# Kernel optimization log

Hardware: AMD Instinct MI355X
Metric: run time of the kernel (lower is better)

Reference implementation:

```python
import jax, jax.numpy as jnp
import numpy as np
import math

B, S, H, NH = 2, 2048, 2048, 16
HD = H // NH
BASE = 10000.0


def _rope_tables():
    inv_freq = 1.0 / (BASE ** (np.arange(0, HD, 2, dtype=np.float32) / HD))
    t = np.arange(S, dtype=np.float32)
    freqs = np.einsum('i,j->ij', t, inv_freq)          # [S, HD/2]
    emb = np.concatenate([freqs, freqs], axis=-1)       # [S, HD]
    return jnp.asarray(np.cos(emb)), jnp.asarray(np.sin(emb))


def setup_inputs() -> dict:
    key = jax.random.key(0)
    ks = jax.random.split(key, 6)
    scale = 1.0 / math.sqrt(H)
    cos, sin = _rope_tables()
    causal = np.triu(np.full((S, S), -1e9, dtype=np.float32), k=1)
    attn_bias = jnp.broadcast_to(jnp.asarray(causal)[None, None], (B, 1, S, S))
    return {
        'hidden_states': jax.random.normal(ks[0], (B, S, H), jnp.float32),
        'masks': jnp.zeros((B, S, S), jnp.float32),
        'attn_bias': attn_bias,
        'cos': cos,
        'sin': sin,
        'wq': jax.random.normal(ks[1], (H, H), jnp.float32) * scale,
        'wk': jax.random.normal(ks[2], (H, H), jnp.float32) * scale,
        'wv': jax.random.normal(ks[3], (H, H), jnp.float32) * scale,
        'wo': jax.random.normal(ks[4], (H, H), jnp.float32) * scale,
        'position_ids': jnp.broadcast_to(jnp.arange(S, dtype=jnp.int64)[None], (B, S)),
    }


def _rotate_half(x):
    x1, x2 = x[..., : x.shape[-1] // 2], x[..., x.shape[-1] // 2:]
    return jnp.concatenate([-x2, x1], axis=-1)


def reference(hidden_states, masks, attn_bias, cos, sin, wq, wk, wv, wo, position_ids):
    b, s, h = hidden_states.shape
    nh, hd = NH, HD
    # QKV projections (torch Linear: x @ W.T), split heads -> [b, nh, s, hd]
    def proj(w):
        return (hidden_states @ w.T).reshape(b, s, nh, hd).transpose(0, 2, 1, 3)
    q, k, v = proj(wq), proj(wk), proj(wv)
    # RoPE
    cos_p = cos[position_ids][:, None]  # [b, 1, s, hd]
    sin_p = sin[position_ids][:, None]
    q = q * cos_p + _rotate_half(q) * sin_p
    k = k * cos_p + _rotate_half(k) * sin_p
    # attention scores with additive masks (mx_attn branch, fp math)
    att = jnp.einsum('bhqd,bhkd->bhqk', q / math.sqrt(hd), k)
    att = att + attn_bias + masks[:, None]
    att = jax.nn.softmax(att, axis=-1)
    out = jnp.einsum('bhqk,bhkd->bhqd', att, v)
    out = out.transpose(0, 2, 1, 3).reshape(b, s, h)
    return out @ wo.T
```

## Files before the change

### kernel.cpp

```cpp
#include <hip/hip_runtime.h>
#include <stdint.h>

#define B_  2
#define S_  2048
#define H_  2048
#define NH_ 16
#define HD_ 128

typedef __bf16 v8bf __attribute__((ext_vector_type(8)));
typedef float  v4f  __attribute__((ext_vector_type(4)));

__device__ __forceinline__ float b2f(unsigned short u) {
  union { unsigned int i; float f; } x; x.i = ((unsigned int)u) << 16; return x.f;
}
__device__ __forceinline__ unsigned short f2b(float f) {
  union { float f; unsigned int i; } x; x.f = f;
  unsigned int r = x.i + 0x7FFFu + ((x.i >> 16) & 1u);
  return (unsigned short)(r >> 16);
}

__device__ __forceinline__ void async16(const void* g, void* l) {
  __builtin_amdgcn_global_load_lds(
      (const __attribute__((address_space(1))) void*)g,
      (__attribute__((address_space(3))) void*)l, 16, 0, 0);
}

__global__ __launch_bounds__(256) void cvt_all(const float* __restrict__ hid,
                                               const float* __restrict__ wq,
                                               const float* __restrict__ wk,
                                               const float* __restrict__ wv,
                                               const float* __restrict__ wo,
                                               unsigned short* __restrict__ Xb,
                                               unsigned short* __restrict__ Wqb,
                                               unsigned short* __restrict__ Wkb,
                                               unsigned short* __restrict__ Wvb,
                                               unsigned short* __restrict__ Wob) {
  int bid = blockIdx.x;
  const float* src;
  unsigned short* dst;
  int rel;
  if (bid < 8192)       { src = hid; dst = Xb;  rel = bid; }
  else if (bid < 12288) { src = wq;  dst = Wqb; rel = bid - 8192; }
  else if (bid < 16384) { src = wk;  dst = Wkb; rel = bid - 12288; }
  else if (bid < 20480) { src = wv;  dst = Wvb; rel = bid - 16384; }
  else                  { src = wo;  dst = Wob; rel = bid - 20480; }
  int i = rel * 256 + threadIdx.x;
  float4 f = *(const float4*)(src + (size_t)i * 4);
  ushort4 u;
  u.x = f2b(f.x); u.y = f2b(f.y); u.z = f2b(f.z); u.w = f2b(f.w);
  *(ushort4*)(dst + (size_t)i * 4) = u;
}

__device__ __forceinline__ void gemm_tile_nt(const unsigned short* __restrict__ A,
                                             const unsigned short* __restrict__ Bm,
                                             int m0, int n0, int Kdim,
                                             unsigned short* As, unsigned short* Bs,
                                             v4f (&acc)[2][8]) {
  const int tid = threadIdx.x;
  const int lane = tid & 63, w = tid >> 6;
  const int lr = lane & 15, lg = lane >> 4;
  const int wm = w * 32;

  for (int k0 = 0; k0 < Kdim; k0 += 32) {
    __syncthreads();
#pragma unroll
    for (int i = 0; i < 2; ++i) {
      const int cbase = i * 256 + w * 64;
      const int cc = cbase + lane;
      const int row = cc >> 2, col = (cc & 3) << 3;
      async16(A  + (size_t)(m0 + row) * Kdim + k0 + col, (char*)As + (size_t)cbase * 16);
      async16(Bm + (size_t)(n0 + row) * Kdim + k0 + col, (char*)Bs + (size_t)cbase * 16);
    }
    __syncthreads();
    v8bf a[2], bb[8];
#pragma unroll
    for (int i = 0; i < 2; i++) a[i]  = *(const v8bf*)(As + (wm + i * 16 + lr) * 32 + lg * 8);
#pragma unroll
    for (int i = 0; i < 8; i++) bb[i] = *(const v8bf*)(Bs + (i * 16 + lr) * 32 + lg * 8);
#pragma unroll
    for (int mi = 0; mi < 2; mi++)
#pragma unroll
      for (int ni = 0; ni < 8; ni++)
        acc[mi][ni] = __builtin_amdgcn_mfma_f32_16x16x32_bf16(a[mi], bb[ni], acc[mi][ni], 0, 0, 0);
  }
}

__global__ __launch_bounds__(256, 2) void gemm_qkv(const unsigned short* __restrict__ X,
                                                   const unsigned short* __restrict__ Wq,
                                                   const unsigned short* __restrict__ Wk,
                                                   const unsigned short* __restrict__ Wv,
                                                   const float* __restrict__ cosT,
                                                   const float* __restrict__ sinT,
                                                   unsigned short* __restrict__ Qo,
                                                   unsigned short* __restrict__ Ko,
                                                   unsigned short* __restrict__ Vt) {
  __shared__ unsigned short As[128 * 32], Bs[128 * 32];
  const int m0 = blockIdx.x * 128;
  const int ny = blockIdx.y;
  const int sel = ny >> 4;
  const int h = ny & 15;
  const unsigned short* Bm = (sel == 0) ? Wq : (sel == 1 ? Wk : Wv);
  const int n0 = h * 128;

  v4f acc[2][8];
#pragma unroll
  for (int i = 0; i < 2; i++)
#pragma unroll
    for (int j = 0; j < 8; j++) { v4f z = {0.f, 0.f, 0.f, 0.f}; acc[i][j] = z; }

  gemm_tile_nt(X, Bm, m0, n0, H_, As, Bs, acc);

  const int lane = threadIdx.x & 63, w = threadIdx.x >> 6;
  const int lr = lane & 15, lg = lane >> 4;
  const int rbase = m0 + w * 32;

  if (sel < 2) {
    unsigned short* Out = (sel == 0) ? Qo : Ko;
    const float sc = (sel == 0) ? (float)(0.08838834764831845 * 1.4426950408889634) : 1.0f;
#pragma unroll
    for (int mi = 0; mi < 2; mi++)
#pragma unroll
      for (int ni = 0; ni < 4; ni++)
#pragma unroll
        for (int r = 0; r < 4; r++) {
          int row = rbase + mi * 16 + lg * 4 + r;
          int s = row & 2047;
          int d = ni * 16 + lr;
          float c  = cosT[(size_t)s * HD_ + d];
          float sn = sinT[(size_t)s * HD_ + d];
          float x1 = acc[mi][ni][r], x2 = acc[mi][ni + 4][r];
          Out[(size_t)row * H_ + n0 + d]      = f2b((x1 * c - x2 * sn) * sc);
          Out[(size_t)row * H_ + n0 + d + 64] = f2b((x2 * c + x1 * sn) * sc);
        }
  } else {
#pragma unroll
    for (int mi = 0; mi < 2; mi++)
#pragma unroll
      for (int ni = 0; ni < 8; ni++) {
        int row0 = rbase + mi * 16 + lg * 4;
        int b = row0 >> 11, s0 = row0 & 2047;
        int d = ni * 16 + lr;
        ushort4 u;
        u.x = f2b(acc[mi][ni][0]); u.y = f2b(acc[mi][ni][1]);
        u.z = f2b(acc[mi][ni][2]); u.w = f2b(acc[mi][ni][3]);
        *(ushort4*)(Vt + ((size_t)((b * NH_ + h) * HD_) + d) * S_ + s0) = u;
      }
  }
}

__global__ __launch_bounds__(256, 2) void gemm_out(const unsigned short* __restrict__ A,
                                                   const unsigned short* __restrict__ Wo,
                                                   float* __restrict__ Out) {
  __shared__ unsigned short As[128 * 32], Bs[128 * 32];
  const int m0 = blockIdx.x * 128;
  const int n0 = blockIdx.y * 128;

  v4f acc[2][8];
#pragma unroll
  for (int i = 0; i < 2; i++)
#pragma unroll
    for (int j = 0; j < 8; j++) { v4f z = {0.f, 0.f, 0.f, 0.f}; acc[i][j] = z; }

  gemm_tile_nt(A, Wo, m0, n0, H_, As, Bs, acc);

  const int lane = threadIdx.x & 63, w = threadIdx.x >> 6;
  const int lr = lane & 15, lg = lane >> 4;
#pragma unroll
  for (int mi = 0; mi < 2; mi++)
#pragma unroll
    for (int ni = 0; ni < 8; ni++)
#pragma unroll
      for (int r = 0; r < 4; r++)
        Out[(size_t)(m0 + w * 32 + mi * 16 + lg * 4 + r) * H_ + n0 + ni * 16 + lr] =
            acc[mi][ni][r];
}

#define KT_ 64

__global__ __launch_bounds__(512, 2) void attn_kernel(const unsigned short* __restrict__ Qb,
                                                      const unsigned short* __restrict__ Kb,
                                                      const unsigned short* __restrict__ Vt,
                                                      unsigned short* __restrict__ Ob) {
  __shared__ __align__(16) char smem[90112];
  unsigned short* Ps = (unsigned short*)(smem + 71680);

  const int tid = threadIdx.x, lane = tid & 63, w = tid >> 6;
  const int lr = lane & 15, lg = lane >> 4;
  const int qp = blockIdx.x, h = blockIdx.y, b = blockIdx.z;

  const int wtile = (w < 4) ? qp : (15 - qp);
  const int wrow = wtile * 128 + (w & 3) * 32;
  const int nkt = (16 - qp) * 2;

  auto stage = [&](int kt, char* Kd) {
    const int k0 = kt * KT_;
    char* Vd = Kd + 17408;
#pragma unroll
    for (int i = 0; i < 3; ++i) {
      int cbase = i * 512 + w * 64;
      if (cbase < 1088) {
        int cc = cbase + lane;
        int row = cc / 17, pos = cc % 17;
        int p2 = (pos == 16) ? 0 : pos;
        async16(Kb + (size_t)(b * S_ + k0 + row) * H_ + h * HD_ + p2 * 8,
                Kd + (size_t)cbase * 16);
      }
    }
#pragma unroll
    for (int i = 0; i < 3; ++i) {
      int cbase = i * 512 + w * 64;
      if (cbase < 1152) {
        int cc = cbase + lane;
        int row = cc / 9, pos = cc % 9;
        int p2 = (pos == 8) ? 0 : pos;
        async16(Vt + ((size_t)((b * NH_ + h) * HD_ + row)) * S_ + k0 + p2 * 8,
                Vd + (size_t)cbase * 16);
      }
    }
  };

  v8bf qf[2][4];
#pragma unroll
  for (int mt = 0; mt < 2; mt++)
#pragma unroll
    for (int ks = 0; ks < 4; ks++)
      qf[mt][ks] = *(const v8bf*)(Qb + (size_t)(b * S_ + wrow + mt * 16 + lr) * H_ +
                                  h * HD_ + ks * 32 + lg * 8);

  v4f o[2][8];
#pragma unroll
  for (int mt = 0; mt < 2; mt++)
#pragma unroll
    for (int nt = 0; nt < 8; nt++) { v4f z = {0.f, 0.f, 0.f, 0.f}; o[mt][nt] = z; }
  float mst[2][4], lst[2][4];
#pragma unroll
  for (int mt = 0; mt < 2; mt++)
#pragma unroll
    for (int r = 0; r < 4; r++) { mst[mt][r] = -1e30f; lst[mt][r] = 0.f; }

  stage(0, smem);
  __syncthreads();

  int cur = 0;
  for (int kt = 0; kt < nkt; kt++) {
    char* curb = smem + cur * 35840;
    if (kt + 1 < nkt) stage(kt + 1, smem + (cur ^ 1) * 35840);

    unsigned short* Ks = (unsigned short*)curb;
    unsigned short* Vs = (unsigned short*)(curb + 17408);
    const int k0 = kt * KT_;

    if (k0 <= wrow + 31) {
      v4f sacc[2][4];
#pragma unroll
      for (int mt = 0; mt < 2; mt++)
#pragma unroll
        for (int nt = 0; nt < 4; nt++) { v4f z = {0.f, 0.f, 0.f, 0.f}; sacc[mt][nt] = z; }
#pragma unroll
      for (int nt = 0; nt < 4; nt++) {
        v8bf kf[4];
#pragma unroll
        for (int ks = 0; ks < 4; ks++)
          kf[ks] = *(const v8bf*)(Ks + (nt * 16 + lr) * 136 + ks * 32 + lg * 8);
#pragma unroll
        for (int mt = 0; mt < 2; mt++)
#pragma unroll
          for (int ks = 0; ks < 4; ks++)
            sacc[mt][nt] =
                __builtin_amdgcn_mfma_f32_16x16x32_bf16(qf[mt][ks], kf[ks], sacc[mt][nt], 0, 0, 0);
      }
      if (k0 + KT_ - 1 > wrow) {
#pragma unroll
        for (int mt = 0; mt < 2; mt++)
#pragma unroll
          for (int nt = 0; nt < 4; nt++)
#pragma unroll
            for (int r = 0; r < 4; r++) {
              int key = k0 + nt * 16 + lr;
              int query = wrow + mt * 16 + lg * 4 + r;
              if (key > query) sacc[mt][nt][r] = -1e30f;
            }
      }
#pragma unroll
      for (int mt = 0; mt < 2; mt++) {
        float rmax[4], alpha[4], rsum[4];
#pragma unroll
        for (int r = 0; r < 4; r++) {
          float v = fmaxf(fmaxf(sacc[mt][0][r], sacc[mt][1][r]),
                          fmaxf(sacc[mt][2][r], sacc[mt][3][r]));
#pragma unroll
          for (int off = 8; off >= 1; off >>= 1) v = fmaxf(v, __shfl_xor(v, off, 64));
          rmax[r] = v;
        }
#pragma unroll
        for (int r = 0; r < 4; r++) {
          float mnew = fmaxf(mst[mt][r], rmax[r]);
          alpha[r] = exp2f(mst[mt][r] - mnew);
          mst[mt][r] = mnew;
          rsum[r] = 0.f;
        }
#pragma unroll
        for (int nt = 0; nt < 4; nt++)
#pragma unroll
          for (int r = 0; r < 4; r++) {
            float p = exp2f(sacc[mt][nt][r] - mst[mt][r]);
            sacc[mt][nt][r] = p;
            rsum[r] += p;
          }
#pragma unroll
        for (int r = 0; r < 4; r++) {
#pragma unroll
          for (int off = 8; off >= 1; off >>= 1) rsum[r] += __shfl_xor(rsum[r], off, 64);
          lst[mt][r] = lst[mt][r] * alpha[r] + rsum[r];
        }
#pragma unroll
        for (int nt = 0; nt < 8; nt++)
#pragma unroll
          for (int r = 0; r < 4; r++) o[mt][nt][r] *= alpha[r];
      }
      v8bf bv[8][2];
#pragma unroll
      for (int nt = 0; nt < 8; nt++)
#pragma unroll
        for (int ks = 0; ks < 2; ks++)
          bv[nt][ks] = *(const v8bf*)(Vs + (nt * 16 + lr) * 72 + ks * 32 + lg * 8);
#pragma unroll
      for (int mt = 0; mt < 2; mt++) {
#pragma unroll
        for (int nt = 0; nt < 4; nt++)
#pragma unroll
          for (int r = 0; r < 4; r++) {
            union { float f; unsigned u; } pu; pu.f = sacc[mt][nt][r];
            Ps[w * 1152 + (lg * 4 + r) * 72 + nt * 16 + lr] =
                (unsigned short)(pu.u >> 16);
          }
        asm volatile("" ::: "memory");
        v8bf af[2];
#pragma unroll
        for (int ks = 0; ks < 2; ks++)
          af[ks] = *(const v8bf*)(Ps + w * 1152 + lr * 72 + ks * 32 + lg * 8);
#pragma unroll
        for (int nt = 0; nt < 8; nt++)
#pragma unroll
          for (int ks = 0; ks < 2; ks++)
            o[mt][nt] = __builtin_amdgcn_mfma_f32_16x16x32_bf16(af[ks], bv[nt][ks], o[mt][nt], 0, 0, 0);
        asm volatile("" ::: "memory");
      }
    }
    __syncthreads();
    cur ^= 1;
  }
#pragma unroll
  for (int mt = 0; mt < 2; mt++) {
    float inv[4];
#pragma unroll
    for (int r = 0; r < 4; r++) inv[r] = 1.f / lst[mt][r];
#pragma unroll
    for (int nt = 0; nt < 8; nt++)
#pragma unroll
      for (int r = 0; r < 4; r++) {
        int row = wrow + mt * 16 + lg * 4 + r;
        int col = h * HD_ + nt * 16 + lr;
        Ob[(size_t)(b * S_ + row) * H_ + col] = f2b(o[mt][nt][r] * inv[r]);
      }
  }
}

extern "C" void kernel_launch(void* const* d_in, const int* in_sizes, int n_in,
                              void* d_out, int out_size, void* d_ws, size_t ws_size,
                              hipStream_t stream) {
  const float* hidden = (const float*)d_in[0];
  const float* cosT = (const float*)d_in[3];
  const float* sinT = (const float*)d_in[4];
  const float* wq = (const float*)d_in[5];
  const float* wk = (const float*)d_in[6];
  const float* wv = (const float*)d_in[7];
  const float* wo = (const float*)d_in[8];
  float* out = (float*)d_out;

  char* p = (char*)d_ws;
  const size_t SZ_X = (size_t)4096 * 2048 * 2;
  const size_t SZ_W = (size_t)2048 * 2048 * 2;
  unsigned short* Xb  = (unsigned short*)p; p += SZ_X;
  unsigned short* Wqb = (unsigned short*)p; p += SZ_W;
  unsigned short* Wkb = (unsigned short*)p; p += SZ_W;
  unsigned short* Wvb = (unsigned short*)p; p += SZ_W;
  unsigned short* Wob = (unsigned short*)p; p += SZ_W;
  unsigned short* Qb  = (unsigned short*)p; p += SZ_X;
  unsigned short* Kb  = (unsigned short*)p; p += SZ_X;
  unsigned short* Vt  = (unsigned short*)p; p += SZ_X;
  unsigned short* Ob  = (unsigned short*)p; p += SZ_X;

  cvt_all<<<24576, 256, 0, stream>>>(hidden, wq, wk, wv, wo, Xb, Wqb, Wkb, Wvb, Wob);
  gemm_qkv<<<dim3(32, 48), 256, 0, stream>>>(Xb, Wqb, Wkb, Wvb, cosT, sinT, Qb, Kb, Vt);
  attn_kernel<<<dim3(8, 16, 2), 512, 0, stream>>>(Qb, Kb, Vt, Ob);
  gemm_out<<<dim3(32, 16), 256, 0, stream>>>(Ob, Wob, out);
}
```

Measured before the change: 448.6 us.

## Rewrite QKV GEMM with 256x256 tiles, double-buffered swizzled LDS, and interleaved MFMA

```diff
diff --git a/kernel.cpp b/kernel.cpp
--- a/kernel.cpp
+++ b/kernel.cpp
@@ -85,7 +85,7 @@
   }
 }
 
-__global__ __launch_bounds__(256, 2) void gemm_qkv(const unsigned short* __restrict__ X,
+__global__ __launch_bounds__(512, 2) void gemm_qkv(const unsigned short* __restrict__ X,
                                                    const unsigned short* __restrict__ Wq,
                                                    const unsigned short* __restrict__ Wk,
                                                    const unsigned short* __restrict__ Wv,
@@ -94,50 +94,151 @@
                                                    unsigned short* __restrict__ Qo,
                                                    unsigned short* __restrict__ Ko,
                                                    unsigned short* __restrict__ Vt) {
-  __shared__ unsigned short As[128 * 32], Bs[128 * 32];
-  const int m0 = blockIdx.x * 128;
+  __shared__ __align__(16) unsigned short lds[4][256 * 64];
+
+  const int tid = threadIdx.x, lane = tid & 63, w = tid >> 6;
+  const int lr = lane & 15, lg = lane >> 4;
+  const int wm = w >> 1, wn = w & 1;
+  const int m0 = blockIdx.x * 256;
   const int ny = blockIdx.y;
-  const int sel = ny >> 4;
-  const int h = ny & 15;
-  const unsigned short* Bm = (sel == 0) ? Wq : (sel == 1 ? Wk : Wv);
-  const int n0 = h * 128;
-
-  v4f acc[2][8];
-#pragma unroll
-  for (int i = 0; i < 2; i++)
+  const int sel = ny >> 3;
+  const int nt = ny & 7;
+  const int n0 = nt * 256;
+  const unsigned short* Bw = (sel == 0) ? Wq : (sel == 1 ? Wk : Wv);
+  const int xsw = (lr & 7) << 3;
+
+  auto stg = [&](const unsigned short* G, int g0, int k0, unsigned short* dst) {
+#pragma unroll
+    for (int i = 0; i < 4; ++i) {
+      const int cbase = i * 512 + w * 64;
+      const int cc = cbase + lane;
+      const int row = cc >> 3;
+      const int kq = (cc & 7) ^ (row & 7);
+      async16(G + (size_t)(g0 + row) * H_ + k0 + kq * 8, (char*)dst + (size_t)cbase * 16);
+    }
+  };
+
+  v4f acc[4][8];
+#pragma unroll
+  for (int i = 0; i < 4; i++)
 #pragma unroll
     for (int j = 0; j < 8; j++) { v4f z = {0.f, 0.f, 0.f, 0.f}; acc[i][j] = z; }
 
-  gemm_tile_nt(X, Bm, m0, n0, H_, As, Bs, acc);
-
-  const int lane = threadIdx.x & 63, w = threadIdx.x >> 6;
-  const int lr = lane & 15, lg = lane >> 4;
-  const int rbase = m0 + w * 32;
-
+  stg(X,  m0, 0, lds[0]);
+  stg(Bw, n0, 0, lds[1]);
+  __syncthreads();
+
+  for (int t = 0; t < 32; ++t) {
+    const unsigned short* As = lds[(t & 1) * 2];
+    const unsigned short* Bs = lds[(t & 1) * 2 + 1];
+    unsigned short* Ad = lds[((t + 1) & 1) * 2];
+    unsigned short* Bd = lds[((t + 1) & 1) * 2 + 1];
+    const int kn = (t + 1) * 64;
+    v8bf bf[8][2], af[2];
+
+    if (t < 31) stg(X, m0, kn, Ad);
+#pragma unroll
+    for (int ni = 0; ni < 8; ni++) {
+      const unsigned short* rp = Bs + (size_t)(wn * 128 + ni * 16 + lr) * 64;
+      bf[ni][0] = *(const v8bf*)(rp + ((lg * 8) ^ xsw));
+      bf[ni][1] = *(const v8bf*)(rp + ((32 + lg * 8) ^ xsw));
+    }
+    {
+      const unsigned short* rp = As + (size_t)(wm * 64 + lr) * 64;
+      af[0] = *(const v8bf*)(rp + ((lg * 8) ^ xsw));
+      af[1] = *(const v8bf*)(rp + ((32 + lg * 8) ^ xsw));
+    }
+    __builtin_amdgcn_s_barrier();
+    asm volatile("s_waitcnt lgkmcnt(0)" ::: "memory");
+    __builtin_amdgcn_sched_barrier(0);
+    __builtin_amdgcn_s_setprio(1);
+#pragma unroll
+    for (int ni = 0; ni < 8; ni++) {
+      acc[0][ni] = __builtin_amdgcn_mfma_f32_16x16x32_bf16(af[0], bf[ni][0], acc[0][ni], 0, 0, 0);
+      acc[0][ni] = __builtin_amdgcn_mfma_f32_16x16x32_bf16(af[1], bf[ni][1], acc[0][ni], 0, 0, 0);
+    }
+    __builtin_amdgcn_s_setprio(0);
+    __builtin_amdgcn_s_barrier();
+
+    if (t < 31) stg(Bw, n0, kn, Bd);
+    {
+      const unsigned short* rp = As + (size_t)(wm * 64 + 16 + lr) * 64;
+      af[0] = *(const v8bf*)(rp + ((lg * 8) ^ xsw));
+      af[1] = *(const v8bf*)(rp + ((32 + lg * 8) ^ xsw));
+    }
+    __builtin_amdgcn_s_barrier();
+    asm volatile("s_waitcnt lgkmcnt(0)" ::: "memory");
+    __builtin_amdgcn_sched_barrier(0);
+    __builtin_amdgcn_s_setprio(1);
+#pragma unroll
+    for (int ni = 0; ni < 8; ni++) {
+      acc[1][ni] = __builtin_amdgcn_mfma_f32_16x16x32_bf16(af[0], bf[ni][0], acc[1][ni], 0, 0, 0);
+      acc[1][ni] = __builtin_amdgcn_mfma_f32_16x16x32_bf16(af[1], bf[ni][1], acc[1][ni], 0, 0, 0);
+    }
+    __builtin_amdgcn_s_setprio(0);
+    __builtin_amdgcn_s_barrier();
+
+    {
+      const unsigned short* rp = As + (size_t)(wm * 64 + 32 + lr) * 64;
+      af[0] = *(const v8bf*)(rp + ((lg * 8) ^ xsw));
+      af[1] = *(const v8bf*)(rp + ((32 + lg * 8) ^ xsw));
+    }
+    __builtin_amdgcn_s_barrier();
+    asm volatile("s_waitcnt lgkmcnt(0)" ::: "memory");
+    __builtin_amdgcn_sched_barrier(0);
+    __builtin_amdgcn_s_setprio(1);
+#pragma unroll
+    for (int ni = 0; ni < 8; ni++) {
+      acc[2][ni] = __builtin_amdgcn_mfma_f32_16x16x32_bf16(af[0], bf[ni][0], acc[2][ni], 0, 0, 0);
+      acc[2][ni] = __builtin_amdgcn_mfma_f32_16x16x32_bf16(af[1], bf[ni][1], acc[2][ni], 0, 0, 0);
+    }
+    __builtin_amdgcn_s_setprio(0);
+    __builtin_amdgcn_s_barrier();
+
+    {
+      const unsigned short* rp = As + (size_t)(wm * 64 + 48 + lr) * 64;
+      af[0] = *(const v8bf*)(rp + ((lg * 8) ^ xsw));
+      af[1] = *(const v8bf*)(rp + ((32 + lg * 8) ^ xsw));
+    }
+    __builtin_amdgcn_s_barrier();
+    asm volatile("s_waitcnt lgkmcnt(0)" ::: "memory");
+    __builtin_amdgcn_sched_barrier(0);
+    __builtin_amdgcn_s_setprio(1);
+#pragma unroll
+    for (int ni = 0; ni < 8; ni++) {
+      acc[3][ni] = __builtin_amdgcn_mfma_f32_16x16x32_bf16(af[0], bf[ni][0], acc[3][ni], 0, 0, 0);
+      acc[3][ni] = __builtin_amdgcn_mfma_f32_16x16x32_bf16(af[1], bf[ni][1], acc[3][ni], 0, 0, 0);
+    }
+    __builtin_amdgcn_s_setprio(0);
+    __syncthreads();
+  }
+
+  const int h = nt * 2 + wn;
+  const int rb0 = m0 + wm * 64;
   if (sel < 2) {
     unsigned short* Out = (sel == 0) ? Qo : Ko;
     const float sc = (sel == 0) ? (float)(0.08838834764831845 * 1.4426950408889634) : 1.0f;
 #pragma unroll
-    for (int mi = 0; mi < 2; mi++)
+    for (int mi = 0; mi < 4; mi++)
 #pragma unroll
       for (int ni = 0; ni < 4; ni++)
 #pragma unroll
         for (int r = 0; r < 4; r++) {
-          int row = rbase + mi * 16 + lg * 4 + r;
+          int row = rb0 + mi * 16 + lg * 4 + r;
           int s = row & 2047;
           int d = ni * 16 + lr;
           float c  = cosT[(size_t)s * HD_ + d];
           float sn = sinT[(size_t)s * HD_ + d];
           float x1 = acc[mi][ni][r], x2 = acc[mi][ni + 4][r];
-          Out[(size_t)row * H_ + n0 + d]      = f2b((x1 * c - x2 * sn) * sc);
-          Out[(size_t)row * H_ + n0 + d + 64] = f2b((x2 * c + x1 * sn) * sc);
+          Out[(size_t)row * H_ + h * HD_ + d]      = f2b((x1 * c - x2 * sn) * sc);
+          Out[(size_t)row * H_ + h * HD_ + d + 64] = f2b((x2 * c + x1 * sn) * sc);
         }
   } else {
 #pragma unroll
-    for (int mi = 0; mi < 2; mi++)
+    for (int mi = 0; mi < 4; mi++)
 #pragma unroll
       for (int ni = 0; ni < 8; ni++) {
-        int row0 = rbase + mi * 16 + lg * 4;
+        int row0 = rb0 + mi * 16 + lg * 4;
         int b = row0 >> 11, s0 = row0 & 2047;
         int d = ni * 16 + lr;
         ushort4 u;
@@ -392,7 +493,7 @@
   unsigned short* Ob  = (unsigned short*)p; p += SZ_X;
 
   cvt_all<<<24576, 256, 0, stream>>>(hidden, wq, wk, wv, wo, Xb, Wqb, Wkb, Wvb, Wob);
-  gemm_qkv<<<dim3(32, 48), 256, 0, stream>>>(Xb, Wqb, Wkb, Wvb, cosT, sinT, Qb, Kb, Vt);
+  gemm_qkv<<<dim3(16, 24), 512, 0, stream>>>(Xb, Wqb, Wkb, Wvb, cosT, sinT, Qb, Kb, Vt);
   attn_kernel<<<dim3(8, 16, 2), 512, 0, stream>>>(Qb, Kb, Vt, Ob);
   gemm_out<<<dim3(32, 16), 256, 0, stream>>>(Ob, Wob, out);
 }
```

After: 457.2 us. About the same (+1.9%).
